# Kernel optimization log

Hardware: AMD Instinct MI355X
Metric: run time of the kernel (lower is better)

The kernel has to match this reference:

```python
import jax, jax.numpy as jnp
import numpy as np

N_TOKENS = 2048
HIDDEN = 1024
INTER = 2816
N_EXPERTS = 8
N_ADAPTERS = 2
MAX_RANK = 16
TOP_K = 2
N_SEQS = 8


def setup_inputs() -> dict:
    key = jax.random.key(0)
    ks = jax.random.split(key, 12)
    f32 = jnp.float32
    std = 0.02
    hidden_states = jax.random.normal(ks[0], (N_TOKENS, HIDDEN), f32)
    topk_ids = jax.random.randint(ks[1], (N_TOKENS, TOP_K), 0, N_EXPERTS)
    tw = jax.random.uniform(ks[2], (N_TOKENS, TOP_K), dtype=f32)
    topk_weights = tw / tw.sum(axis=-1, keepdims=True)
    gate_a = jax.random.normal(ks[3], (N_ADAPTERS, N_EXPERTS, MAX_RANK, HIDDEN), f32) * std
    gate_b = jax.random.normal(ks[4], (N_ADAPTERS, N_EXPERTS, INTER, MAX_RANK), f32) * std
    up_a = jax.random.normal(ks[5], (N_ADAPTERS, N_EXPERTS, MAX_RANK, HIDDEN), f32) * std
    up_b = jax.random.normal(ks[6], (N_ADAPTERS, N_EXPERTS, INTER, MAX_RANK), f32) * std
    down_a = jax.random.normal(ks[7], (N_ADAPTERS, N_EXPERTS, MAX_RANK, INTER), f32) * std
    down_b = jax.random.normal(ks[8], (N_ADAPTERS, N_EXPERTS, HIDDEN, MAX_RANK), f32) * std
    weight_indices = jax.random.randint(ks[9], (N_SEQS,), 0, N_ADAPTERS)
    seq_lens = jnp.full((N_SEQS,), N_TOKENS // N_SEQS, dtype=jnp.int32)
    lora_ranks = jnp.array([16, 8], dtype=jnp.int32)
    scalings = jnp.array([2.0, 1.0], dtype=f32)
    base_gate_up_weight = jax.random.normal(ks[10], (N_EXPERTS, 2 * INTER, HIDDEN), f32) * std
    base_down_weight = jax.random.normal(ks[11], (N_EXPERTS, HIDDEN, INTER), f32) * std
    return {
        'hidden_states': hidden_states, 'topk_ids': topk_ids, 'topk_weights': topk_weights,
        'gate_a': gate_a, 'gate_b': gate_b, 'up_a': up_a, 'up_b': up_b,
        'down_a': down_a, 'down_b': down_b, 'weight_indices': weight_indices,
        'seq_lens': seq_lens, 'lora_ranks': lora_ranks, 'scalings': scalings,
        'base_gate_up_weight': base_gate_up_weight, 'base_down_weight': base_down_weight,
    }


def _forward(hidden_states, topk_ids, topk_weights, gate_a, gate_b, up_a, up_b,
             down_a, down_b, weight_indices, seq_lens, lora_ranks, scalings,
             base_gate_up_weight, base_down_weight):
    N, H = hidden_states.shape
    A, E, R, _ = gate_a.shape
    I = gate_b.shape[2]
    x = hidden_states.astype(jnp.float32)
    # token -> sequence -> adapter (replaces the per-token python loop)
    token_to_seq = jnp.searchsorted(jnp.cumsum(seq_lens), jnp.arange(N), side='right')
    adapter = weight_indices[token_to_seq]                               # [N]
    scale_t = scalings[adapter].astype(jnp.float32)[:, None]             # [N,1]
    # per-adapter rank truncation A[:rank] == zeroing rows r >= rank of LoRA-A
    rmask = (jnp.arange(R)[None, :] < lora_ranks[:, None]).astype(jnp.float32)  # [A,R]
    ga = gate_a.astype(jnp.float32) * rmask[:, None, :, None]
    ua = up_a.astype(jnp.float32) * rmask[:, None, :, None]
    da = down_a.astype(jnp.float32) * rmask[:, None, :, None]
    gb = gate_b.astype(jnp.float32)
    ub = up_b.astype(jnp.float32)
    db = down_b.astype(jnp.float32)
    # low-rank input projections for all adapters & experts (tiny: N*A*E*R)
    z_gate = jnp.einsum('nh,aerh->naer', x, ga)
    z_up = jnp.einsum('nh,aerh->naer', x, ua)
    sel = adapter[:, None, None]
    Wgu = base_gate_up_weight.astype(jnp.float32)   # [E, 2I, H]
    Wd = base_down_weight.astype(jnp.float32)       # [E, H, I]
    out = jnp.zeros((N, H), jnp.float32)
    for e in range(E):
        # summed routing weight for this expert per token (0 => no contribution)
        w_e = jnp.where(topk_ids == e, topk_weights, 0.0).sum(axis=1).astype(jnp.float32)  # [N]
        base_gate = x @ Wgu[e, :I].T                 # [N,I]
        base_up = x @ Wgu[e, I:].T                   # [N,I]
        lg = jnp.take_along_axis(jnp.einsum('nar,air->nai', z_gate[:, :, e], gb[:, e]), sel, axis=1)[:, 0]
        lu = jnp.take_along_axis(jnp.einsum('nar,air->nai', z_up[:, :, e], ub[:, e]), sel, axis=1)[:, 0]
        gate_out = base_gate + scale_t * lg
        up_out = base_up + scale_t * lu
        act = jax.nn.silu(gate_out) * up_out         # [N,I]
        zd = jnp.einsum('ni,ari->nar', act, da[:, e])
        ld = jnp.take_along_axis(jnp.einsum('nar,ahr->nah', zd, db[:, e]), sel, axis=1)[:, 0]
        base_down = act @ Wd[e].T                    # [N,H]
        out = out + w_e[:, None] * (base_down + scale_t * ld)
    return out.astype(hidden_states.dtype)


def reference(hidden_states, topk_ids, topk_weights, gate_a, gate_b, up_a, up_b,
              down_a, down_b, weight_indices, seq_lens, lora_ranks, scalings,
              base_gate_up_weight, base_down_weight):
    return _forward(hidden_states, topk_ids, topk_weights, gate_a, gate_b, up_a, up_b,
                    down_a, down_b, weight_indices, seq_lens, lora_ranks, scalings,
                    base_gate_up_weight, base_down_weight)
```

## Files before the change

kernel.cpp:

```cpp
#include <hip/hip_runtime.h>
#include <hip/hip_bf16.h>
#include <math.h>

#define N_TOK   2048
#define HIDDEN  1024
#define INTER   2816
#define NEXP    8
#define NADAPT  2
#define MAXRANK 16
#define TOPK    2
#define NSEQ    8
#define NPAIRS  (N_TOK*TOPK)
#define NGU     (2*INTER)

typedef unsigned short u16;
typedef __attribute__((ext_vector_type(8))) short bf16x8;
typedef __attribute__((ext_vector_type(4))) float f32x4;

#define F_CNT   0u
#define F_PERM  4096u
#define F_ZG    139264u
#define F_ZU    401408u
#define F_ZD    663552u
#define F_XBF   1048576u
#define F_ACT   5242880u
#define F_GB    28311552u
#define F_UB    29753344u
#define F_DB    31195136u
#define F_GA_BF 31719424u
#define F_UA_BF 32243712u
#define F_ZDF   32768000u
#define F_WGU   33554432u
#define F_WD    125829120u
#define F_DA_BF F_XBF
#define FAST_NEED 171966464u

#define B_CNT   0u
#define B_PERM  4096u
#define B_ZG    262144u
#define B_ZU    524288u
#define B_ZD    786432u
#define B_ACT   1048576u

__device__ __forceinline__ float bf2f(u16 u){
  union { unsigned int i; float f; } v; v.i = ((unsigned int)u)<<16; return v.f;
}
__device__ __forceinline__ u16 f2bf(float f){
  union { float f; unsigned int i; } v; v.f = f;
  unsigned int i = v.i;
  return (u16)((i + 0x7fffu + ((i>>16)&1u)) >> 16);
}
__device__ __forceinline__ uint4 cvt8(const float* src){
  float4 lo = *(const float4*)src;
  float4 hi = *(const float4*)(src+4);
  uint4 r;
  r.x = (unsigned)f2bf(lo.x) | ((unsigned)f2bf(lo.y)<<16);
  r.y = (unsigned)f2bf(lo.z) | ((unsigned)f2bf(lo.w)<<16);
  r.z = (unsigned)f2bf(hi.x) | ((unsigned)f2bf(hi.y)<<16);
  r.w = (unsigned)f2bf(hi.z) | ((unsigned)f2bf(hi.w)<<16);
  return r;
}
__device__ __forceinline__ uint2 cvt4(float4 v){
  uint2 r;
  r.x = (unsigned)f2bf(v.x) | ((unsigned)f2bf(v.y)<<16);
  r.y = (unsigned)f2bf(v.z) | ((unsigned)f2bf(v.w)<<16);
  return r;
}

__device__ __forceinline__ void cvt_chunk8k(const float* __restrict__ src, u16* __restrict__ dst, int c, int t){
  size_t b4 = (size_t)c*2048 + t;
  float4 v0 = ((const float4*)src)[b4];
  float4 v1 = ((const float4*)src)[b4 + 256];
  float4 v2 = ((const float4*)src)[b4 + 512];
  float4 v3 = ((const float4*)src)[b4 + 768];
  float4 v4 = ((const float4*)src)[b4 + 1024];
  float4 v5 = ((const float4*)src)[b4 + 1280];
  float4 v6 = ((const float4*)src)[b4 + 1536];
  float4 v7 = ((const float4*)src)[b4 + 1792];
  ((uint2*)dst)[b4]        = cvt4(v0);
  ((uint2*)dst)[b4 + 256]  = cvt4(v1);
  ((uint2*)dst)[b4 + 512]  = cvt4(v2);
  ((uint2*)dst)[b4 + 768]  = cvt4(v3);
  ((uint2*)dst)[b4 + 1024] = cvt4(v4);
  ((uint2*)dst)[b4 + 1280] = cvt4(v5);
  ((uint2*)dst)[b4 + 1536] = cvt4(v6);
  ((uint2*)dst)[b4 + 1792] = cvt4(v7);
}
__device__ __forceinline__ void zero_chunk8k(float* dst, int c, int t){
  size_t b4 = (size_t)c*2048 + t;
  #pragma unroll
  for (int i = 0; i < 8; ++i)
    ((float4*)dst)[b4 + i*256] = make_float4(0.f,0.f,0.f,0.f);
}

__device__ __forceinline__ void gl16(const void* g, void* l){
  __builtin_amdgcn_global_load_lds(
      (const __attribute__((address_space(1))) unsigned int*)g,
      (__attribute__((address_space(3))) unsigned int*)l, 16, 0, 0);
}

__device__ __forceinline__ int token_adapter(int n, const int* seq_lens, const int* widx){
  int cum = 0;
  #pragma unroll
  for (int s = 0; s < NSEQ; ++s){ cum += seq_lens[s]; if (n < cum) return widx[s]; }
  return widx[NSEQ-1];
}

__global__ void k_zero(float* outf, int* cnt, float* zdf){
  int t = threadIdx.x;
  if (blockIdx.x < 2048){
    int id = blockIdx.x*256 + t;
    *(float4*)&outf[(size_t)id*4] = make_float4(0.f,0.f,0.f,0.f);
  } else {
    int id = (blockIdx.x - 2048)*256 + t;
    *(float4*)&zdf[(size_t)id*4] = make_float4(0.f,0.f,0.f,0.f);
  }
  if (blockIdx.x == 0 && t < NEXP) cnt[t] = 0;
}

__global__ void k_route(const int* __restrict__ topk_ids, int* cnt, int* perm){
  int p = blockIdx.x*256 + threadIdx.x;
  if (p >= NPAIRS) return;
  int e = topk_ids[p];
  int pos = atomicAdd(&cnt[e], 1);
  perm[e*NPAIRS + pos] = p;
}

__global__ void k_cvt(const float* __restrict__ src, u16* __restrict__ dst, int n4){
  int id = blockIdx.x*256 + threadIdx.x;
  if (id >= n4) return;
  ((uint2*)dst)[id] = cvt4(((const float4*)src)[id]);
}

__global__ void k_prep(
    const float* __restrict__ x,  const float* __restrict__ gb, const float* __restrict__ ub,
    const float* __restrict__ ga, const float* __restrict__ ua, const float* __restrict__ db_,
    u16* xb, u16* gbb, u16* ubb, u16* gab, u16* uab, u16* dbb,
    float* outf, float* zdf, int* cnt)
{
  int b = blockIdx.x, t = threadIdx.x;
  if (b == 0 && t < NEXP) cnt[t] = 0;
  if      (b < 256) cvt_chunk8k(x,   xb,  b,       t);
  else if (b < 344) cvt_chunk8k(gb,  gbb, b - 256, t);
  else if (b < 432) cvt_chunk8k(ub,  ubb, b - 344, t);
  else if (b < 464) cvt_chunk8k(ga,  gab, b - 432, t);
  else if (b < 496) cvt_chunk8k(ua,  uab, b - 464, t);
  else if (b < 528) cvt_chunk8k(db_, dbb, b - 496, t);
  else if (b < 784) zero_chunk8k(outf, b - 528, t);
  else              zero_chunk8k(zdf,  b - 784, t);
}

__global__ __launch_bounds__(256) void k_zgu_plus(
    const u16* __restrict__ xb, const u16* __restrict__ gab, const u16* __restrict__ uab,
    const float* __restrict__ wgu_f32, u16* __restrict__ wgub,
    const int* __restrict__ cnt, const int* __restrict__ perm,
    const int* __restrict__ widx, const int* __restrict__ seq_lens,
    const int* __restrict__ ranks, const float* __restrict__ scal,
    u16* __restrict__ zg, u16* __restrict__ zu)
{
  int bx = blockIdx.x, t = threadIdx.x;
  if (bx >= 64){
    int c = blockIdx.y*704 + (bx - 64);
    cvt_chunk8k(wgu_f32, wgub, c, t);
    return;
  }
  int e = blockIdx.y;
  int me = cnt[e];
  int tm = bx;
  if (tm*64 >= me) return;

  __shared__ __align__(16) u16 As[64*32];
  __shared__ __align__(16) u16 Bs[64*32];

  int r0 = t >> 2;
  int kc = ((t&3) - r0) & 3;
  int ko = kc*8;
  int mg = tm*64 + r0;
  int pa = perm[e*NPAIRS + min(mg, me-1)];
  const u16* arow = xb + (size_t)(pa>>1)*HIDDEN + ko;
  int jr = r0 & 31;
  const u16* brow = (r0 < 32 ? gab : uab)
                    + (size_t)(((jr>>4)*NEXP + e)*MAXRANK + (jr&15))*HIDDEN + ko;

  int wv = t>>6, lane = t&63;
  u16* Asw = &As[wv*512];
  u16* Bsw = &Bs[wv*512];
  int wm = wv>>1, wn = wv&1;
  int l15 = lane&15, q = lane>>4;

  f32x4 acc[2][2] = {};
  int aoff[2], boff[2];
  #pragma unroll
  for (int i=0;i<2;++i){ int row = wm*32 + i*16 + l15; aoff[i] = row*32 + ((q+row)&3)*8; }
  #pragma unroll
  for (int j=0;j<2;++j){ int row = wn*32 + j*16 + l15; boff[j] = row*32 + ((q+row)&3)*8; }

  for (int kt = 0; kt < HIDDEN/32; ++kt){
    __syncthreads();
    gl16(arow + kt*32, Asw);
    gl16(brow + kt*32, Bsw);
    __syncthreads();
    bf16x8 af[2], bfr[2];
    #pragma unroll
    for (int i=0;i<2;++i) af[i] = *(const bf16x8*)&As[aoff[i]];
    #pragma unroll
    for (int j=0;j<2;++j) bfr[j] = *(const bf16x8*)&Bs[boff[j]];
    #pragma unroll
    for (int i=0;i<2;++i)
      #pragma unroll
      for (int j=0;j<2;++j)
        acc[i][j] = __builtin_amdgcn_mfma_f32_16x16x32_bf16(af[i], bfr[j], acc[i][j],0,0,0);
  }

  u16* dstz = wn ? zu : zg;
  #pragma unroll
  for (int i=0;i<2;++i){
    #pragma unroll
    for (int r=0;r<4;++r){
      int mgo = tm*64 + wm*32 + i*16 + q*4 + r;
      if (mgo < me){
        int p = perm[e*NPAIRS + mgo];
        int a = token_adapter(p>>1, seq_lens, widx);
        int rank = ranks[a]; float sc = scal[a];
        #pragma unroll
        for (int j=0;j<2;++j){
          int jc = j*16 + l15;
          float v = ((jc>>4)==a && (jc&15)<rank) ? sc*acc[i][j][r] : 0.f;
          dstz[(size_t)p*32 + jc] = f2bf(v);
        }
      }
    }
  }
}

__global__ __launch_bounds__(256) void k_zd_mfma(
    const u16* __restrict__ act, const u16* __restrict__ dab,
    const int* __restrict__ cnt, const int* __restrict__ perm,
    const int* __restrict__ widx, const int* __restrict__ seq_lens,
    const int* __restrict__ ranks, const float* __restrict__ scal,
    float* __restrict__ zdf)
{
  int e = blockIdx.z;
  int me = cnt[e];
  int tm = blockIdx.y;
  if (tm*64 >= me) return;
  int ks = blockIdx.x;
  int t = threadIdx.x;

  __shared__ __align__(16) u16 As[64*32];
  __shared__ __align__(16) u16 Bs[32*32];

  int r0 = t >> 2;
  int kc = ((t&3) - r0) & 3;
  int ko = kc*8;
  int mg = tm*64 + r0;
  int pa = perm[e*NPAIRS + min(mg, me-1)];
  const u16* arow = act + (size_t)pa*INTER + ko;
  int jr = r0 & 31;
  const u16* brow = dab + (size_t)(((jr>>4)*NEXP + e)*MAXRANK + (jr&15))*INTER + ko;

  int wv = t>>6, lane = t&63;
  u16* Asw = &As[wv*512];
  u16* Bsw = &Bs[(wv&1)*512];
  int l15 = lane&15, q = lane>>4;

  f32x4 acc[2] = {};
  int aoff; { int row = wv*16 + l15; aoff = row*32 + ((q+row)&3)*8; }
  int boff[2];
  #pragma unroll
  for (int j=0;j<2;++j){ int row = j*16 + l15; boff[j] = row*32 + ((q+row)&3)*8; }

  int kt0 = ks*22, kt1 = kt0 + 22;
  for (int kt = kt0; kt < kt1; ++kt){
    __syncthreads();
    gl16(arow + kt*32, Asw);
    if (wv < 2) gl16(brow + kt*32, Bsw);
    __syncthreads();
    bf16x8 af = *(const bf16x8*)&As[aoff];
    bf16x8 b0 = *(const bf16x8*)&Bs[boff[0]];
    bf16x8 b1 = *(const bf16x8*)&Bs[boff[1]];
    acc[0] = __builtin_amdgcn_mfma_f32_16x16x32_bf16(af, b0, acc[0],0,0,0);
    acc[1] = __builtin_amdgcn_mfma_f32_16x16x32_bf16(af, b1, acc[1],0,0,0);
  }

  #pragma unroll
  for (int r=0;r<4;++r){
    int mgo = tm*64 + wv*16 + q*4 + r;
    if (mgo < me){
      int p = perm[e*NPAIRS + mgo];
      int a = token_adapter(p>>1, seq_lens, widx);
      int rank = ranks[a]; float sc = scal[a];
      #pragma unroll
      for (int j=0;j<2;++j){
        int jc = j*16 + l15;
        if ((jc>>4)==a && (jc&15)<rank)
          atomicAdd(&zdf[(size_t)p*32 + jc], sc*acc[j][r]);
      }
    }
  }
}

__global__ __launch_bounds__(256) void k_zgu(
    const float* __restrict__ x, const int* __restrict__ topk_ids,
    const float* __restrict__ gate_a, const float* __restrict__ up_a,
    const int* __restrict__ widx, const int* __restrict__ seq_lens,
    const int* __restrict__ ranks, const float* __restrict__ scal,
    u16* __restrict__ zg, u16* __restrict__ zu)
{
  int p = blockIdx.x, n = p >> 1, t = threadIdx.x;
  int e = topk_ids[p];
  __shared__ float xs[HIDDEN];
  for (int i = t; i < HIDDEN; i += 256) xs[i] = x[(size_t)n*HIDDEN + i];
  if (t < 32){ zg[p*32 + t] = 0; zu[p*32 + t] = 0; }
  __syncthreads();
  int a = token_adapter(n, seq_lens, widx);
  int rank = ranks[a];
  float scale = scal[a];
  int wv = t >> 6, lane = t & 63;
  for (int i = 0; i < 8; ++i){
    int o = wv*8 + i;
    int r = o & 15;
    const float* wrow = ((o < 16) ? gate_a : up_a) + (size_t)((a*NEXP + e)*MAXRANK + r)*HIDDEN;
    float s = 0.f;
    for (int h = lane; h < HIDDEN; h += 64) s += xs[h] * wrow[h];
    s += __shfl_down(s,32); s += __shfl_down(s,16); s += __shfl_down(s,8);
    s += __shfl_down(s,4);  s += __shfl_down(s,2);  s += __shfl_down(s,1);
    if (lane == 0 && r < rank)
      (o < 16 ? zg : zu)[p*32 + a*16 + r] = f2bf(scale * s);
  }
}

__global__ __launch_bounds__(256) void k_zd(
    const u16* __restrict__ act, const int* __restrict__ topk_ids,
    const float* __restrict__ down_a,
    const int* __restrict__ widx, const int* __restrict__ seq_lens,
    const int* __restrict__ ranks, const float* __restrict__ scal,
    u16* __restrict__ zd)
{
  int p = blockIdx.x, n = p >> 1, t = threadIdx.x;
  int e = topk_ids[p];
  __shared__ float as_[INTER];
  for (int i = t; i < INTER; i += 256) as_[i] = bf2f(act[(size_t)p*INTER + i]);
  if (t < 32) zd[p*32 + t] = 0;
  __syncthreads();
  int a = token_adapter(n, seq_lens, widx);
  int rank = ranks[a];
  float scale = scal[a];
  int wv = t >> 6, lane = t & 63;
  for (int i = 0; i < 4; ++i){
    int r = wv*4 + i;
    const float* wrow = down_a + (size_t)((a*NEXP + e)*MAXRANK + r)*INTER;
    float s = 0.f;
    for (int h = lane; h < INTER; h += 64) s += as_[h] * wrow[h];
    s += __shfl_down(s,32); s += __shfl_down(s,16); s += __shfl_down(s,8);
    s += __shfl_down(s,4);  s += __shfl_down(s,2);  s += __shfl_down(s,1);
    if (lane == 0 && r < rank) zd[p*32 + a*16 + r] = f2bf(scale * s);
  }
}

__global__ __launch_bounds__(256) void k_gufused_plus(
    const u16* __restrict__ xb, const u16* __restrict__ wgu,
    const u16* __restrict__ gbb, const u16* __restrict__ ubb,
    const u16* __restrict__ zg, const u16* __restrict__ zu,
    const float* __restrict__ wd_f32, u16* __restrict__ wdb_out,
    const int* __restrict__ cnt, const int* __restrict__ perm,
    u16* __restrict__ act)
{
  int tn = blockIdx.x;
  int t = threadIdx.x;
  if (tn >= 44){
    int c = (tn - 44)*256 + (blockIdx.z*32 + blockIdx.y);
    if (c < 2816) cvt_chunk8k(wd_f32, wdb_out, c, t);
    return;
  }
  int e = blockIdx.z;
  int me = cnt[e];
  int tm = blockIdx.y;
  if (tm*128 >= me) return;

  __shared__ __align__(16) u16 As[128*32];
  __shared__ __align__(16) u16 Bg[64*32];
  __shared__ __align__(16) u16 Bu[64*32];

  int r0 = t >> 2;
  int kc = ((t&3) - r0) & 3;
  int ko = kc*8;
  int mg0 = tm*128 + r0, mg1 = mg0 + 64;
  int p0 = perm[e*NPAIRS + min(mg0, me-1)];
  int p1 = perm[e*NPAIRS + min(mg1, me-1)];
  const u16* arow0 = xb + (size_t)(p0>>1)*HIDDEN + ko;
  const u16* arow1 = xb + (size_t)(p1>>1)*HIDDEN + ko;
  int jg = tn*64 + r0;
  const u16* browg = wgu + ((size_t)e*NGU + jg)*HIDDEN + ko;
  const u16* browu = wgu + ((size_t)e*NGU + INTER + jg)*HIDDEN + ko;

  int wvb = (t>>6)*512;
  u16* Asw0 = &As[wvb];
  u16* Asw1 = &As[2048 + wvb];
  u16* Bgw  = &Bg[wvb];
  u16* Buw  = &Bu[wvb];

  int wv = t>>6, lane = t&63;
  int wm = wv>>1, wn = wv&1;
  int l15 = lane&15, q = lane>>4;

  f32x4 accg[4][2] = {};
  f32x4 accu[4][2] = {};
  int aoff[4], boff[2];
  #pragma unroll
  for (int i=0;i<4;++i){ int row = wm*64 + i*16 + l15; aoff[i] = row*32 + ((q+row)&3)*8; }
  #pragma unroll
  for (int j=0;j<2;++j){ int row = wn*32 + j*16 + l15; boff[j] = row*32 + ((q+row)&3)*8; }

  for (int kt = 0; kt < HIDDEN/32; ++kt){
    __syncthreads();
    gl16(arow0 + kt*32, Asw0);
    gl16(arow1 + kt*32, Asw1);
    gl16(browg + kt*32, Bgw);
    gl16(browu + kt*32, Buw);
    __syncthreads();
    bf16x8 af[4], bgf[2], buf[2];
    #pragma unroll
    for (int i=0;i<4;++i) af[i] = *(const bf16x8*)&As[aoff[i]];
    #pragma unroll
    for (int j=0;j<2;++j){ bgf[j] = *(const bf16x8*)&Bg[boff[j]]; buf[j] = *(const bf16x8*)&Bu[boff[j]]; }
    #pragma unroll
    for (int i=0;i<4;++i)
      #pragma unroll
      for (int j=0;j<2;++j){
        accg[i][j] = __builtin_amdgcn_mfma_f32_16x16x32_bf16(af[i], bgf[j], accg[i][j],0,0,0);
        accu[i][j] = __builtin_amdgcn_mfma_f32_16x16x32_bf16(af[i], buf[j], accu[i][j],0,0,0);
      }
  }
  {
    int aid = kc>>1, rr = (kc&1)*8;
    const u16* gB = gbb + ((size_t)(aid*NEXP+e)*INTER + jg)*MAXRANK + rr;
    const u16* uB = ubb + ((size_t)(aid*NEXP+e)*INTER + jg)*MAXRANK + rr;
    __syncthreads();
    gl16(zg + (size_t)p0*32 + ko, Asw0);
    gl16(zg + (size_t)p1*32 + ko, Asw1);
    gl16(gB, Bgw);
    __syncthreads();
    {
      bf16x8 af[4], bgf[2];
      #pragma unroll
      for (int i=0;i<4;++i) af[i] = *(const bf16x8*)&As[aoff[i]];
      #pragma unroll
      for (int j=0;j<2;++j) bgf[j] = *(const bf16x8*)&Bg[boff[j]];
      #pragma unroll
      for (int i=0;i<4;++i)
        #pragma unroll
        for (int j=0;j<2;++j)
          accg[i][j] = __builtin_amdgcn_mfma_f32_16x16x32_bf16(af[i], bgf[j], accg[i][j],0,0,0);
    }
    __syncthreads();
    gl16(zu + (size_t)p0*32 + ko, Asw0);
    gl16(zu + (size_t)p1*32 + ko, Asw1);
    gl16(uB, Bgw);
    __syncthreads();
    {
      bf16x8 af[4], buf[2];
      #pragma unroll
      for (int i=0;i<4;++i) af[i] = *(const bf16x8*)&As[aoff[i]];
      #pragma unroll
      for (int j=0;j<2;++j) buf[j] = *(const bf16x8*)&Bg[boff[j]];
      #pragma unroll
      for (int i=0;i<4;++i)
        #pragma unroll
        for (int j=0;j<2;++j)
          accu[i][j] = __builtin_amdgcn_mfma_f32_16x16x32_bf16(af[i], buf[j], accu[i][j],0,0,0);
    }
  }

  int col = l15, quad = q;
  #pragma unroll
  for (int i = 0; i < 4; ++i){
    #pragma unroll
    for (int r = 0; r < 4; ++r){
      int mg = tm*128 + wm*64 + i*16 + quad*4 + r;
      if (mg < me){
        int p = perm[e*NPAIRS + mg];
        size_t base = (size_t)p*INTER;
        #pragma unroll
        for (int j = 0; j < 2; ++j){
          int jc = tn*64 + wn*32 + j*16 + col;
          float g = accg[i][j][r], u = accu[i][j][r];
          float s = g / (1.f + __expf(-g));
          act[base + jc] = f2bf(s*u);
        }
      }
    }
  }
}

__global__ __launch_bounds__(256) void k_down_bf(
    const u16* __restrict__ act, const u16* __restrict__ wdb,
    const u16* __restrict__ dbb, const u16* __restrict__ zd,
    const float* __restrict__ tw,
    const int* __restrict__ cnt, const int* __restrict__ perm,
    float* __restrict__ outf)
{
  int e = blockIdx.z;
  int me = cnt[e];
  int tm = blockIdx.y;
  if (tm*128 >= me) return;
  int tn = blockIdx.x & 7;
  int ks = blockIdx.x >> 3;
  int t = threadIdx.x;

  __shared__ __align__(16) u16 As[128*32];
  __shared__ __align__(16) u16 Bs[128*32];

  int r0 = t >> 2;
  int kc = ((t&3) - r0) & 3;
  int ko = kc*8;
  int mg0 = tm*128 + r0, mg1 = mg0 + 64;
  int p0 = perm[e*NPAIRS + min(mg0, me-1)];
  int p1 = perm[e*NPAIRS + min(mg1, me-1)];
  const u16* arow0 = act + (size_t)p0*INTER + ko;
  const u16* arow1 = act + (size_t)p1*INTER + ko;
  int j0 = tn*128 + r0, j1 = j0 + 64;
  const u16* brow0 = wdb + ((size_t)e*HIDDEN + j0)*INTER + ko;
  const u16* brow1 = wdb + ((size_t)e*HIDDEN + j1)*INTER + ko;

  int wvb = (t>>6)*512;
  u16* Asw0 = &As[wvb];
  u16* Asw1 = &As[2048 + wvb];
  u16* Bsw0 = &Bs[wvb];
  u16* Bsw1 = &Bs[2048 + wvb];

  int wv = t>>6, lane = t&63;
  int wm = wv>>1, wn = wv&1;
  int l15 = lane&15, q = lane>>4;

  f32x4 acc[4][4] = {};
  int aoff[4], boff[4];
  #pragma unroll
  for (int i=0;i<4;++i){ int row = wm*64 + i*16 + l15; aoff[i] = row*32 + ((q+row)&3)*8; }
  #pragma unroll
  for (int j=0;j<4;++j){ int row = wn*64 + j*16 + l15; boff[j] = row*32 + ((q+row)&3)*8; }

  auto mma = [&](){
    bf16x8 af[4], bfr[4];
    #pragma unroll
    for (int i=0;i<4;++i){ af[i] = *(const bf16x8*)&As[aoff[i]]; bfr[i] = *(const bf16x8*)&Bs[boff[i]]; }
    #pragma unroll
    for (int i=0;i<4;++i)
      #pragma unroll
      for (int j=0;j<4;++j)
        acc[i][j] = __builtin_amdgcn_mfma_f32_16x16x32_bf16(af[i], bfr[j], acc[i][j],0,0,0);
  };

  int kt0 = ks*22, kt1 = kt0 + 22;
  for (int kt = kt0; kt < kt1; ++kt){
    __syncthreads();
    gl16(arow0 + kt*32, Asw0);
    gl16(arow1 + kt*32, Asw1);
    gl16(brow0 + kt*32, Bsw0);
    gl16(brow1 + kt*32, Bsw1);
    __syncthreads();
    mma();
  }
  if (ks == 3){
    int aid = kc>>1, rr = (kc&1)*8;
    __syncthreads();
    gl16(zd + (size_t)p0*32 + ko, Asw0);
    gl16(zd + (size_t)p1*32 + ko, Asw1);
    gl16(dbb + ((size_t)(aid*NEXP+e)*HIDDEN + j0)*MAXRANK + rr, Bsw0);
    gl16(dbb + ((size_t)(aid*NEXP+e)*HIDDEN + j1)*MAXRANK + rr, Bsw1);
    __syncthreads();
    mma();
  }

  int col = l15, quad = q;
  #pragma unroll
  for (int i = 0; i < 4; ++i){
    #pragma unroll
    for (int r = 0; r < 4; ++r){
      int mg = tm*128 + wm*64 + i*16 + quad*4 + r;
      if (mg < me){
        int p = perm[e*NPAIRS + mg];
        float wp = tw[p];
        size_t base = (size_t)(p >> 1)*HIDDEN;
        #pragma unroll
        for (int j = 0; j < 4; ++j){
          int jc = tn*128 + wn*64 + j*16 + col;
          atomicAdd(&outf[base + jc], wp * acc[i][j][r]);
        }
      }
    }
  }
}

__global__ __launch_bounds__(256) void k_gufused(
    const float* __restrict__ x, const float* __restrict__ wgu,
    const float* __restrict__ gate_b, const float* __restrict__ up_b,
    const u16* __restrict__ zg, const u16* __restrict__ zu,
    const int* __restrict__ cnt, const int* __restrict__ perm,
    u16* __restrict__ act)
{
  int e = blockIdx.z;
  int me = cnt[e];
  int tm = blockIdx.y;
  if (tm*128 >= me) return;
  int tn = blockIdx.x;
  int t = threadIdx.x;

  __shared__ __align__(16) u16 As[128*32];
  __shared__ __align__(16) u16 Bg[64*32];
  __shared__ __align__(16) u16 Bu[64*32];

  int r0 = t >> 2, cc = t & 3;
  int mg0 = tm*128 + r0, mg1 = mg0 + 64;
  int p0 = perm[e*NPAIRS + min(mg0, me-1)];
  int p1 = perm[e*NPAIRS + min(mg1, me-1)];
  const float* arow0 = x + (size_t)(p0 >> 1)*HIDDEN;
  const float* arow1 = x + (size_t)(p1 >> 1)*HIDDEN;
  int jg = tn*64 + r0;
  const float* browg = wgu + ((size_t)e*NGU + jg)*HIDDEN;
  const float* browu = wgu + ((size_t)e*NGU + INTER + jg)*HIDDEN;

  int wv = t >> 6, lane = t & 63;
  int wm = wv >> 1, wn = wv & 1;

  f32x4 accg[4][2] = {};
  f32x4 accu[4][2] = {};
  int aoff[4], boff[2];
  #pragma unroll
  for (int i = 0; i < 4; ++i) aoff[i] = (wm*64 + i*16 + (lane&15))*32 + (lane>>4)*8;
  #pragma unroll
  for (int j = 0; j < 2; ++j) boff[j] = (wn*32 + j*16 + (lane&15))*32 + (lane>>4)*8;

  for (int kt = 0; kt < HIDDEN/32; ++kt){
    uint4 a0 = cvt8(arow0 + kt*32 + cc*8);
    uint4 a1 = cvt8(arow1 + kt*32 + cc*8);
    uint4 bg = cvt8(browg + kt*32 + cc*8);
    uint4 bu = cvt8(browu + kt*32 + cc*8);
    __syncthreads();
    *(uint4*)&As[r0*32 + cc*8]      = a0;
    *(uint4*)&As[(r0+64)*32 + cc*8] = a1;
    *(uint4*)&Bg[r0*32 + cc*8]      = bg;
    *(uint4*)&Bu[r0*32 + cc*8]      = bu;
    __syncthreads();
    bf16x8 af[4], bgf[2], buf[2];
    #pragma unroll
    for (int i = 0; i < 4; ++i) af[i] = *(const bf16x8*)&As[aoff[i]];
    #pragma unroll
    for (int j = 0; j < 2; ++j){ bgf[j] = *(const bf16x8*)&Bg[boff[j]]; buf[j] = *(const bf16x8*)&Bu[boff[j]]; }
    #pragma unroll
    for (int i = 0; i < 4; ++i)
      #pragma unroll
      for (int j = 0; j < 2; ++j){
        accg[i][j] = __builtin_amdgcn_mfma_f32_16x16x32_bf16(af[i], bgf[j], accg[i][j], 0, 0, 0);
        accu[i][j] = __builtin_amdgcn_mfma_f32_16x16x32_bf16(af[i], buf[j], accu[i][j], 0, 0, 0);
      }
  }
  {
    uint4 a0 = *(const uint4*)(zg + (size_t)p0*32 + cc*8);
    uint4 a1 = *(const uint4*)(zg + (size_t)p1*32 + cc*8);
    int aid = cc >> 1, rr = (cc & 1)*8;
    uint4 bg = cvt8(gate_b + ((size_t)(aid*NEXP + e)*INTER + jg)*MAXRANK + rr);
    __syncthreads();
    *(uint4*)&As[r0*32 + cc*8]      = a0;
    *(uint4*)&As[(r0+64)*32 + cc*8] = a1;
    *(uint4*)&Bg[r0*32 + cc*8]      = bg;
    __syncthreads();
    bf16x8 af[4], bgf[2];
    #pragma unroll
    for (int i = 0; i < 4; ++i) af[i] = *(const bf16x8*)&As[aoff[i]];
    #pragma unroll
    for (int j = 0; j < 2; ++j) bgf[j] = *(const bf16x8*)&Bg[boff[j]];
    #pragma unroll
    for (int i = 0; i < 4; ++i)
      #pragma unroll
      for (int j = 0; j < 2; ++j)
        accg[i][j] = __builtin_amdgcn_mfma_f32_16x16x32_bf16(af[i], bgf[j], accg[i][j], 0, 0, 0);
  }
  {
    uint4 a0 = *(const uint4*)(zu + (size_t)p0*32 + cc*8);
    uint4 a1 = *(const uint4*)(zu + (size_t)p1*32 + cc*8);
    int aid = cc >> 1, rr = (cc & 1)*8;
    uint4 bu = cvt8(up_b + ((size_t)(aid*NEXP + e)*INTER + jg)*MAXRANK + rr);
    __syncthreads();
    *(uint4*)&As[r0*32 + cc*8]      = a0;
    *(uint4*)&As[(r0+64)*32 + cc*8] = a1;
    *(uint4*)&Bg[r0*32 + cc*8]      = bu;
    __syncthreads();
    bf16x8 af[4], buf[2];
    #pragma unroll
    for (int i = 0; i < 4; ++i) af[i] = *(const bf16x8*)&As[aoff[i]];
    #pragma unroll
    for (int j = 0; j < 2; ++j) buf[j] = *(const bf16x8*)&Bg[boff[j]];
    #pragma unroll
    for (int i = 0; i < 4; ++i)
      #pragma unroll
      for (int j = 0; j < 2; ++j)
        accu[i][j] = __builtin_amdgcn_mfma_f32_16x16x32_bf16(af[i], buf[j], accu[i][j], 0, 0, 0);
  }
  int col = lane & 15, quad = lane >> 4;
  #pragma unroll
  for (int i = 0; i < 4; ++i){
    #pragma unroll
    for (int r = 0; r < 4; ++r){
      int mg = tm*128 + wm*64 + i*16 + quad*4 + r;
      if (mg < me){
        int p = perm[e*NPAIRS + mg];
        size_t base = (size_t)p*INTER;
        #pragma unroll
        for (int j = 0; j < 2; ++j){
          int jc = tn*64 + wn*32 + j*16 + col;
          float g = accg[i][j][r], u = accu[i][j][r];
          float s = g / (1.f + __expf(-g));
          act[base + jc] = f2bf(s*u);
        }
      }
    }
  }
}

__global__ __launch_bounds__(256) void k_gemm_down(
    const u16* __restrict__ act, const float* __restrict__ wd,
    const float* __restrict__ down_b, const u16* __restrict__ zd,
    const float* __restrict__ tw,
    const int* __restrict__ cnt, const int* __restrict__ perm,
    float* __restrict__ outf)
{
  int e = blockIdx.z;
  int me = cnt[e];
  int tm = blockIdx.y;
  if (tm*128 >= me) return;
  int tn = blockIdx.x;
  int t = threadIdx.x;

  __shared__ __align__(16) u16 As[128*32];
  __shared__ __align__(16) u16 Bs[128*32];

  int r0 = t >> 2, cc = t & 3;
  int mg0 = tm*128 + r0, mg1 = mg0 + 64;
  int p0 = perm[e*NPAIRS + min(mg0, me-1)];
  int p1 = perm[e*NPAIRS + min(mg1, me-1)];
  const u16* arow0 = act + (size_t)p0*INTER;
  const u16* arow1 = act + (size_t)p1*INTER;
  int j0 = tn*128 + r0, j1 = j0 + 64;
  const float* brow0 = wd + ((size_t)e*HIDDEN + j0)*INTER;
  const float* brow1 = wd + ((size_t)e*HIDDEN + j1)*INTER;

  int wv = t >> 6, lane = t & 63;
  int wm = wv >> 1, wn = wv & 1;

  f32x4 acc[4][4] = {};
  int aoff[4], boff[4];
  #pragma unroll
  for (int i = 0; i < 4; ++i){
    aoff[i] = (wm*64 + i*16 + (lane&15))*32 + (lane>>4)*8;
    boff[i] = (wn*64 + i*16 + (lane&15))*32 + (lane>>4)*8;
  }

  auto compute = [&](){
    bf16x8 af[4], bfr[4];
    #pragma unroll
    for (int i = 0; i < 4; ++i){
      af[i]  = *(const bf16x8*)&As[aoff[i]];
      bfr[i] = *(const bf16x8*)&Bs[boff[i]];
    }
    #pragma unroll
    for (int i = 0; i < 4; ++i)
      #pragma unroll
      for (int j = 0; j < 4; ++j)
        acc[i][j] = __builtin_amdgcn_mfma_f32_16x16x32_bf16(af[i], bfr[j], acc[i][j], 0, 0, 0);
  };

  for (int kt = 0; kt < INTER/32; ++kt){
    uint4 a0 = *(const uint4*)(arow0 + kt*32 + cc*8);
    uint4 a1 = *(const uint4*)(arow1 + kt*32 + cc*8);
    uint4 b0 = cvt8(brow0 + kt*32 + cc*8);
    uint4 b1 = cvt8(brow1 + kt*32 + cc*8);
    __syncthreads();
    *(uint4*)&As[r0*32 + cc*8]      = a0;
    *(uint4*)&As[(r0+64)*32 + cc*8] = a1;
    *(uint4*)&Bs[r0*32 + cc*8]      = b0;
    *(uint4*)&Bs[(r0+64)*32 + cc*8] = b1;
    __syncthreads();
    compute();
  }
  {
    uint4 a0 = *(const uint4*)(zd + (size_t)p0*32 + cc*8);
    uint4 a1 = *(const uint4*)(zd + (size_t)p1*32 + cc*8);
    int aid = cc >> 1, rr = (cc & 1)*8;
    uint4 b0 = cvt8(down_b + ((size_t)(aid*NEXP + e)*HIDDEN + j0)*MAXRANK + rr);
    uint4 b1 = cvt8(down_b + ((size_t)(aid*NEXP + e)*HIDDEN + j1)*MAXRANK + rr);
    __syncthreads();
    *(uint4*)&As[r0*32 + cc*8]      = a0;
    *(uint4*)&As[(r0+64)*32 + cc*8] = a1;
    *(uint4*)&Bs[r0*32 + cc*8]      = b0;
    *(uint4*)&Bs[(r0+64)*32 + cc*8] = b1;
    __syncthreads();
    compute();
  }
  int col = lane & 15, quad = lane >> 4;
  #pragma unroll
  for (int i = 0; i < 4; ++i){
    #pragma unroll
    for (int r = 0; r < 4; ++r){
      int mg = tm*128 + wm*64 + i*16 + quad*4 + r;
      if (mg < me){
        int p = perm[e*NPAIRS + mg];
        float wp = tw[p];
        size_t base = (size_t)(p >> 1)*HIDDEN;
        #pragma unroll
        for (int j = 0; j < 4; ++j){
          int jc = tn*128 + wn*64 + j*16 + col;
          atomicAdd(&outf[base + jc], wp * acc[i][j][r]);
        }
      }
    }
  }
}

extern "C" void kernel_launch(void* const* d_in, const int* in_sizes, int n_in,
                              void* d_out, int out_size, void* d_ws, size_t ws_size,
                              hipStream_t stream){
  const float* x        = (const float*)d_in[0];
  const int*   topk_ids = (const int*)d_in[1];
  const float* tw       = (const float*)d_in[2];
  const float* gate_a   = (const float*)d_in[3];
  const float* gate_b   = (const float*)d_in[4];
  const float* up_a     = (const float*)d_in[5];
  const float* up_b     = (const float*)d_in[6];
  const float* down_a   = (const float*)d_in[7];
  const float* down_b   = (const float*)d_in[8];
  const int*   widx     = (const int*)d_in[9];
  const int*   seq_lens = (const int*)d_in[10];
  const int*   ranks    = (const int*)d_in[11];
  const float* scal     = (const float*)d_in[12];
  const float* wgu      = (const float*)d_in[13];
  const float* wd       = (const float*)d_in[14];
  float* outf = (float*)d_out;
  char* ws = (char*)d_ws;

  if (ws_size >= (size_t)FAST_NEED){
    int* cnt  = (int*)(ws + F_CNT);
    int* perm = (int*)(ws + F_PERM);
    u16* zg   = (u16*)(ws + F_ZG);
    u16* zu   = (u16*)(ws + F_ZU);
    u16* zd   = (u16*)(ws + F_ZD);
    u16* xb   = (u16*)(ws + F_XBF);
    u16* act  = (u16*)(ws + F_ACT);
    u16* gbb  = (u16*)(ws + F_GB);
    u16* ubb  = (u16*)(ws + F_UB);
    u16* dbb  = (u16*)(ws + F_DB);
    u16* gab  = (u16*)(ws + F_GA_BF);
    u16* uab  = (u16*)(ws + F_UA_BF);
    float* zdf= (float*)(ws + F_ZDF);
    u16* dab  = (u16*)(ws + F_DA_BF);
    u16* wgub = (u16*)(ws + F_WGU);
    u16* wdb  = (u16*)(ws + F_WD);

    hipLaunchKernelGGL(k_prep, dim3(800), dim3(256), 0, stream,
                       x, gate_b, up_b, gate_a, up_a, down_b,
                       xb, gbb, ubb, gab, uab, dbb, outf, zdf, cnt);
    hipLaunchKernelGGL(k_route, dim3(16), dim3(256), 0, stream, topk_ids, cnt, perm);
    hipLaunchKernelGGL(k_zgu_plus, dim3(64 + 704, NEXP), dim3(256), 0, stream,
                       xb, gab, uab, wgu, wgub, cnt, perm, widx, seq_lens, ranks, scal, zg, zu);
    hipLaunchKernelGGL(k_gufused_plus, dim3(44 + 11, 32, NEXP), dim3(256), 0, stream,
                       xb, wgub, gbb, ubb, zg, zu, wd, wdb, cnt, perm, act);
    hipLaunchKernelGGL(k_cvt, dim3((NADAPT*NEXP*MAXRANK*INTER/4+255)/256), dim3(256), 0, stream,
                       down_a, dab, NADAPT*NEXP*MAXRANK*INTER/4);
    hipLaunchKernelGGL(k_zd_mfma, dim3(4, 64, NEXP), dim3(256), 0, stream,
                       act, dab, cnt, perm, widx, seq_lens, ranks, scal, zdf);
    hipLaunchKernelGGL(k_cvt, dim3((NPAIRS*32/4+255)/256), dim3(256), 0, stream,
                       zdf, zd, NPAIRS*32/4);
    hipLaunchKernelGGL(k_down_bf, dim3(32, 32, NEXP), dim3(256), 0, stream,
                       act, wdb, dbb, zd, tw, cnt, perm, outf);
  } else {
    int* cnt  = (int*)(ws + B_CNT);
    int* perm = (int*)(ws + B_PERM);
    u16* zg   = (u16*)(ws + B_ZG);
    u16* zu   = (u16*)(ws + B_ZU);
    u16* zd   = (u16*)(ws + B_ZD);
    u16* act  = (u16*)(ws + B_ACT);

    hipLaunchKernelGGL(k_zero,  dim3(2048), dim3(256), 0, stream, outf, cnt, outf);
    hipLaunchKernelGGL(k_route, dim3(16), dim3(256), 0, stream, topk_ids, cnt, perm);
    hipLaunchKernelGGL(k_zgu,   dim3(NPAIRS), dim3(256), 0, stream,
                       x, topk_ids, gate_a, up_a, widx, seq_lens, ranks, scal, zg, zu);
    hipLaunchKernelGGL(k_gufused, dim3(INTER/64, 32, NEXP), dim3(256), 0, stream,
                       x, wgu, gate_b, up_b, zg, zu, cnt, perm, act);
    hipLaunchKernelGGL(k_zd,    dim3(NPAIRS), dim3(256), 0, stream,
                       act, topk_ids, down_a, widx, seq_lens, ranks, scal, zd);
    hipLaunchKernelGGL(k_gemm_down, dim3(HIDDEN/128, 32, NEXP), dim3(256), 0, stream,
                       act, wd, down_b, zd, tw, cnt, perm, outf);
  }
}
```

Before: 621.8 us.

## Read fp32 expert weights directly in GEMMs instead of pre-converting to bf16

```diff
diff --git a/kernel.cpp b/kernel.cpp
--- a/kernel.cpp
+++ b/kernel.cpp
@@ -30,9 +30,7 @@
 #define F_GA_BF 31719424u
 #define F_UA_BF 32243712u
 #define F_ZDF   32768000u
-#define F_WGU   33554432u
-#define F_WD    125829120u
-#define F_DA_BF F_XBF
+#define F_DA_BF 33554432u
 #define FAST_NEED 171966464u
 
 #define B_CNT   0u
@@ -135,7 +133,8 @@
 __global__ void k_prep(
     const float* __restrict__ x,  const float* __restrict__ gb, const float* __restrict__ ub,
     const float* __restrict__ ga, const float* __restrict__ ua, const float* __restrict__ db_,
-    u16* xb, u16* gbb, u16* ubb, u16* gab, u16* uab, u16* dbb,
+    const float* __restrict__ da,
+    u16* xb, u16* gbb, u16* ubb, u16* gab, u16* uab, u16* dbb, u16* dab,
     float* outf, float* zdf, int* cnt)
 {
   int b = blockIdx.x, t = threadIdx.x;
@@ -146,28 +145,23 @@
   else if (b < 464) cvt_chunk8k(ga,  gab, b - 432, t);
   else if (b < 496) cvt_chunk8k(ua,  uab, b - 464, t);
   else if (b < 528) cvt_chunk8k(db_, dbb, b - 496, t);
-  else if (b < 784) zero_chunk8k(outf, b - 528, t);
-  else              zero_chunk8k(zdf,  b - 784, t);
-}
-
-__global__ __launch_bounds__(256) void k_zgu_plus(
+  else if (b < 616) cvt_chunk8k(da,  dab, b - 528, t);
+  else if (b < 872) zero_chunk8k(outf, b - 616, t);
+  else              zero_chunk8k(zdf,  b - 872, t);
+}
+
+__global__ __launch_bounds__(256) void k_zgu_mfma(
     const u16* __restrict__ xb, const u16* __restrict__ gab, const u16* __restrict__ uab,
-    const float* __restrict__ wgu_f32, u16* __restrict__ wgub,
     const int* __restrict__ cnt, const int* __restrict__ perm,
     const int* __restrict__ widx, const int* __restrict__ seq_lens,
     const int* __restrict__ ranks, const float* __restrict__ scal,
     u16* __restrict__ zg, u16* __restrict__ zu)
 {
-  int bx = blockIdx.x, t = threadIdx.x;
-  if (bx >= 64){
-    int c = blockIdx.y*704 + (bx - 64);
-    cvt_chunk8k(wgu_f32, wgub, c, t);
-    return;
-  }
   int e = blockIdx.y;
   int me = cnt[e];
-  int tm = bx;
+  int tm = blockIdx.x;
   if (tm*64 >= me) return;
+  int t = threadIdx.x;
 
   __shared__ __align__(16) u16 As[64*32];
   __shared__ __align__(16) u16 Bs[64*32];
@@ -358,25 +352,19 @@
   }
 }
 
-__global__ __launch_bounds__(256) void k_gufused_plus(
-    const u16* __restrict__ xb, const u16* __restrict__ wgu,
+__global__ __launch_bounds__(256) void k_gu_f32(
+    const u16* __restrict__ xb, const float* __restrict__ wgu_f32,
     const u16* __restrict__ gbb, const u16* __restrict__ ubb,
     const u16* __restrict__ zg, const u16* __restrict__ zu,
-    const float* __restrict__ wd_f32, u16* __restrict__ wdb_out,
     const int* __restrict__ cnt, const int* __restrict__ perm,
     u16* __restrict__ act)
 {
-  int tn = blockIdx.x;
-  int t = threadIdx.x;
-  if (tn >= 44){
-    int c = (tn - 44)*256 + (blockIdx.z*32 + blockIdx.y);
-    if (c < 2816) cvt_chunk8k(wd_f32, wdb_out, c, t);
-    return;
-  }
   int e = blockIdx.z;
   int me = cnt[e];
   int tm = blockIdx.y;
   if (tm*128 >= me) return;
+  int tn = blockIdx.x;
+  int t = threadIdx.x;
 
   __shared__ __align__(16) u16 As[128*32];
   __shared__ __align__(16) u16 Bg[64*32];
@@ -391,14 +379,13 @@
   const u16* arow0 = xb + (size_t)(p0>>1)*HIDDEN + ko;
   const u16* arow1 = xb + (size_t)(p1>>1)*HIDDEN + ko;
   int jg = tn*64 + r0;
-  const u16* browg = wgu + ((size_t)e*NGU + jg)*HIDDEN + ko;
-  const u16* browu = wgu + ((size_t)e*NGU + INTER + jg)*HIDDEN + ko;
+  const float* browg = wgu_f32 + ((size_t)e*NGU + jg)*HIDDEN + ko;
+  const float* browu = wgu_f32 + ((size_t)e*NGU + INTER + jg)*HIDDEN + ko;
 
   int wvb = (t>>6)*512;
   u16* Asw0 = &As[wvb];
   u16* Asw1 = &As[2048 + wvb];
   u16* Bgw  = &Bg[wvb];
-  u16* Buw  = &Bu[wvb];
 
   int wv = t>>6, lane = t&63;
   int wm = wv>>1, wn = wv&1;
@@ -413,11 +400,13 @@
   for (int j=0;j<2;++j){ int row = wn*32 + j*16 + l15; boff[j] = row*32 + ((q+row)&3)*8; }
 
   for (int kt = 0; kt < HIDDEN/32; ++kt){
+    uint4 bg = cvt8(browg + kt*32);
+    uint4 bu = cvt8(browu + kt*32);
     __syncthreads();
     gl16(arow0 + kt*32, Asw0);
     gl16(arow1 + kt*32, Asw1);
-    gl16(browg + kt*32, Bgw);
-    gl16(browu + kt*32, Buw);
+    *(uint4*)&Bg[wvb + lane*8] = bg;
+    *(uint4*)&Bu[wvb + lane*8] = bu;
     __syncthreads();
     bf16x8 af[4], bgf[2], buf[2];
     #pragma unroll
@@ -493,8 +482,8 @@
   }
 }
 
-__global__ __launch_bounds__(256) void k_down_bf(
-    const u16* __restrict__ act, const u16* __restrict__ wdb,
+__global__ __launch_bounds__(256) void k_down_f32(
+    const u16* __restrict__ act, const float* __restrict__ wd_f32,
     const u16* __restrict__ dbb, const u16* __restrict__ zd,
     const float* __restrict__ tw,
     const int* __restrict__ cnt, const int* __restrict__ perm,
@@ -520,8 +509,8 @@
   const u16* arow0 = act + (size_t)p0*INTER + ko;
   const u16* arow1 = act + (size_t)p1*INTER + ko;
   int j0 = tn*128 + r0, j1 = j0 + 64;
-  const u16* brow0 = wdb + ((size_t)e*HIDDEN + j0)*INTER + ko;
-  const u16* brow1 = wdb + ((size_t)e*HIDDEN + j1)*INTER + ko;
+  const float* brow0 = wd_f32 + ((size_t)e*HIDDEN + j0)*INTER + ko;
+  const float* brow1 = wd_f32 + ((size_t)e*HIDDEN + j1)*INTER + ko;
 
   int wvb = (t>>6)*512;
   u16* Asw0 = &As[wvb];
@@ -553,11 +542,13 @@
 
   int kt0 = ks*22, kt1 = kt0 + 22;
   for (int kt = kt0; kt < kt1; ++kt){
+    uint4 b0 = cvt8(brow0 + kt*32);
+    uint4 b1 = cvt8(brow1 + kt*32);
     __syncthreads();
     gl16(arow0 + kt*32, Asw0);
     gl16(arow1 + kt*32, Asw1);
-    gl16(brow0 + kt*32, Bsw0);
-    gl16(brow1 + kt*32, Bsw1);
+    *(uint4*)&Bs[wvb + lane*8]        = b0;
+    *(uint4*)&Bs[2048 + wvb + lane*8] = b1;
     __syncthreads();
     mma();
   }
@@ -853,25 +844,21 @@
     u16* uab  = (u16*)(ws + F_UA_BF);
     float* zdf= (float*)(ws + F_ZDF);
     u16* dab  = (u16*)(ws + F_DA_BF);
-    u16* wgub = (u16*)(ws + F_WGU);
-    u16* wdb  = (u16*)(ws + F_WD);
-
-    hipLaunchKernelGGL(k_prep, dim3(800), dim3(256), 0, stream,
-                       x, gate_b, up_b, gate_a, up_a, down_b,
-                       xb, gbb, ubb, gab, uab, dbb, outf, zdf, cnt);
+
+    hipLaunchKernelGGL(k_prep, dim3(888), dim3(256), 0, stream,
+                       x, gate_b, up_b, gate_a, up_a, down_b, down_a,
+                       xb, gbb, ubb, gab, uab, dbb, dab, outf, zdf, cnt);
     hipLaunchKernelGGL(k_route, dim3(16), dim3(256), 0, stream, topk_ids, cnt, perm);
-    hipLaunchKernelGGL(k_zgu_plus, dim3(64 + 704, NEXP), dim3(256), 0, stream,
-                       xb, gab, uab, wgu, wgub, cnt, perm, widx, seq_lens, ranks, scal, zg, zu);
-    hipLaunchKernelGGL(k_gufused_plus, dim3(44 + 11, 32, NEXP), dim3(256), 0, stream,
-                       xb, wgub, gbb, ubb, zg, zu, wd, wdb, cnt, perm, act);
-    hipLaunchKernelGGL(k_cvt, dim3((NADAPT*NEXP*MAXRANK*INTER/4+255)/256), dim3(256), 0, stream,
-                       down_a, dab, NADAPT*NEXP*MAXRANK*INTER/4);
+    hipLaunchKernelGGL(k_zgu_mfma, dim3(64, NEXP), dim3(256), 0, stream,
+                       xb, gab, uab, cnt, perm, widx, seq_lens, ranks, scal, zg, zu);
+    hipLaunchKernelGGL(k_gu_f32, dim3(INTER/64, 32, NEXP), dim3(256), 0, stream,
+                       xb, wgu, gbb, ubb, zg, zu, cnt, perm, act);
     hipLaunchKernelGGL(k_zd_mfma, dim3(4, 64, NEXP), dim3(256), 0, stream,
                        act, dab, cnt, perm, widx, seq_lens, ranks, scal, zdf);
     hipLaunchKernelGGL(k_cvt, dim3((NPAIRS*32/4+255)/256), dim3(256), 0, stream,
                        zdf, zd, NPAIRS*32/4);
-    hipLaunchKernelGGL(k_down_bf, dim3(32, 32, NEXP), dim3(256), 0, stream,
-                       act, wdb, dbb, zd, tw, cnt, perm, outf);
+    hipLaunchKernelGGL(k_down_f32, dim3(32, 32, NEXP), dim3(256), 0, stream,
+                       act, wd, dbb, zd, tw, cnt, perm, outf);
   } else {
     int* cnt  = (int*)(ws + B_CNT);
     int* perm = (int*)(ws + B_PERM);
```

Result: faster. 591.8 us (-4.8%).
